# Optimization experiments

Measured on AMD Instinct MI355X. Metric: run time of the kernel, lower is better.

The kernel has to match this reference:

```python
import jax, jax.numpy as jnp
import numpy as np

NUM_CLASSES = 10
PGD_NUMS = 10
ALPHA = 0.15
# Hardcoded in the original module: sign vector for 10 classes
SIGN_VEC = jnp.array([-1.0] * 4 + [1.0] * 6, dtype=jnp.float32)


def setup_inputs() -> dict:
    key = jax.random.key(0)
    k1, k2, k3 = jax.random.split(key, 3)
    B = 1048576
    logit = jax.random.normal(k1, (B, NUM_CLASSES), dtype=jnp.float32)
    y = jax.random.randint(k2, (B,), 0, NUM_CLASSES, dtype=jnp.int32)
    label_freq = jax.random.randint(k3, (NUM_CLASSES,), 0, PGD_NUMS, dtype=jnp.int32)
    return {"logit": logit, "y": y, "label_freq": label_freq}


def _compute_adv(logit, y):
    # softmax over classes, then per-class mean of softmax rows (one-hot^T @ p)
    p = jax.nn.softmax(logit, axis=-1)  # [B, C]
    sum_class_logit = jax.ops.segment_sum(p, y, num_segments=NUM_CLASSES)  # [C, C]
    counts = jax.ops.segment_sum(jnp.ones(y.shape[0], dtype=logit.dtype), y,
                                 num_segments=NUM_CLASSES)  # [C]
    counts = jnp.where(counts == 0, jnp.asarray(100.0, logit.dtype), counts)
    mean_class_logit = sum_class_logit / counts[:, None]  # [C, C]
    grad = mean_class_logit - jnp.eye(NUM_CLASSES, dtype=logit.dtype)
    # Faithful to torch: norm over dim=0 (columns), then reshape(-1,1) divides row i
    col_norm = jnp.linalg.norm(grad, axis=0)  # [C]
    grad = grad / col_norm[:, None]
    grad = ALPHA * grad * SIGN_VEC[:, None].astype(logit.dtype)
    return grad[y]  # index_select along dim 0 -> [B, C]


def reference(logit, y, label_freq):
    logit_copy = logit

    def step(l, _):
        l_new = l + _compute_adv(l, y)
        return l_new, l_new

    _, logit_steps = jax.lax.scan(step, logit, None, length=PGD_NUMS)  # [P, B, C]

    # Original: logit_news = sum_i logit_steps[label_freq[i]] * (y == i)
    # Since class masks are disjoint, this is a per-sample gather of step label_freq[y[n]].
    steps_per_sample = label_freq[y]  # [B]
    B = logit.shape[0]
    logit_news = logit_steps[steps_per_sample, jnp.arange(B)]  # [B, C]

    # mean cross-entropy
    log_p = jax.nn.log_softmax(logit_news, axis=-1)
    loss_adv = -jnp.mean(jnp.take_along_axis(log_p, y[:, None].astype(jnp.int32), axis=1))
    return loss_adv, logit_news, logit_copy
```

## Files before the change

### kernel.cpp

```cpp
#include <hip/hip_runtime.h>

#define PGD   10
#define ALPHA 0.15f
#define NTAB  32
#define NTHR  256
#define TSAMP 1024
#define NSUB  8

#define WS_COUNTS 0
#define WS_STAB   320
#define WS_DGLOB  32320
#define WS_ZERO_N 33320

__global__ void k_init(float* __restrict__ ws, float* __restrict__ out) {
    int i = blockIdx.x * blockDim.x + threadIdx.x;
    if (i == 0) out[0] = 0.f;
    int gs = gridDim.x * blockDim.x;
    for (int k = i; k < WS_ZERO_N; k += gs) ws[k] = 0.f;
}

__device__ __forceinline__ void table_phase(
    const float* __restrict__ Sg, const float* __restrict__ counts_tab,
    const float* __restrict__ Dprev,
    float* shT, float* shCnt, float* shCn, float* shD_out, int tid)
{
    if (tid < 10) {
        float s = 0.f;
        #pragma unroll
        for (int k = 0; k < NTAB; ++k) s += counts_tab[k * 10 + tid];
        shCnt[tid] = (s == 0.f) ? 100.f : s;
    }
    if (tid < 100) {
        float s = 0.f;
        #pragma unroll
        for (int k = 0; k < NTAB; ++k) s += Sg[k * 100 + tid];
        shT[tid] = s;
    }
    __syncthreads();
    if (tid < 100) {
        int c = tid / 10, j = tid - c * 10;
        shT[tid] = shT[tid] / shCnt[c] - ((c == j) ? 1.f : 0.f);
    }
    __syncthreads();
    if (tid < 10) {
        float s = 0.f;
        for (int cc = 0; cc < 10; ++cc) { float g = shT[cc * 10 + tid]; s += g * g; }
        shCn[tid] = sqrtf(s);
    }
    __syncthreads();
    if (tid < 100) {
        int c = tid / 10;
        float sign = (c < 4) ? -1.f : 1.f;
        float g = shT[tid] / shCn[c] * (ALPHA * sign);
        shD_out[tid] = (Dprev ? Dprev[tid] : 0.f) + g;
    }
    __syncthreads();
}

__device__ __forceinline__ void load_tile(const float* __restrict__ logit,
                                          const int* __restrict__ y,
                                          size_t fbase, size_t ftot, int B,
                                          int tid, int blk, float4 q[10], int4& yq)
{
    #pragma unroll
    for (int i = 0; i < 10; ++i) {
        size_t fi = fbase + (size_t)(tid + i * NTHR) * 4;
        if (fi + 4 <= ftot) {
            q[i] = *reinterpret_cast<const float4*>(logit + fi);
        } else {
            float e[4];
            #pragma unroll
            for (int e2 = 0; e2 < 4; ++e2) e[e2] = (fi + e2 < ftot) ? logit[fi + e2] : 0.f;
            q[i] = make_float4(e[0], e[1], e[2], e[3]);
        }
    }
    int yi = blk * TSAMP + tid * 4;
    if (yi + 4 <= B) {
        yq = *reinterpret_cast<const int4*>(y + yi);
    } else {
        yq.x = (yi     < B) ? y[yi]     : 0;
        yq.y = (yi + 1 < B) ? y[yi + 1] : 0;
        yq.z = (yi + 2 < B) ? y[yi + 2] : 0;
        yq.w = (yi + 3 < B) ? y[yi + 3] : 0;
    }
}

__global__ __launch_bounds__(NTHR) void k_step(
    const float* __restrict__ logit, const int* __restrict__ y,
    float* __restrict__ ws, int B, int t )
{
    __shared__ float tile[TSAMP * 10];
    __shared__ int   yt[TSAMP];
    __shared__ float wtab[NSUB][100];
    __shared__ float ctab[NSUB][10];
    __shared__ float sh_D[100];
    __shared__ float shT[100];
    __shared__ float shCnt[10];
    __shared__ float shCn[10];

    const int tid = threadIdx.x;

    float* counts_tab = ws + WS_COUNTS;
    float* S_tab      = ws + WS_STAB;
    float* D_glob     = ws + WS_DGLOB;

    const size_t fbase = (size_t)blockIdx.x * (TSAMP * 10);
    const size_t ftot  = (size_t)B * 10;
    float4 q[10];
    int4 yq;
    load_tile(logit, y, fbase, ftot, B, tid, blockIdx.x, q, yq);

    for (int i = tid; i < NSUB * 100; i += NTHR) (&wtab[0][0])[i] = 0.f;
    if (t == 1) for (int i = tid; i < NSUB * 10; i += NTHR) (&ctab[0][0])[i] = 0.f;

    if (t >= 2) {
        table_phase(S_tab + (size_t)(t - 2) * (NTAB * 100), counts_tab,
                    (t >= 3) ? (D_glob + (size_t)(t - 3) * 100) : nullptr,
                    shT, shCnt, shCn, sh_D, tid);
        if (blockIdx.x == 0 && tid < 100) D_glob[(size_t)(t - 2) * 100 + tid] = sh_D[tid];
    }

    float4* tp = reinterpret_cast<float4*>(tile);
    #pragma unroll
    for (int i = 0; i < 10; ++i) tp[tid + i * NTHR] = q[i];
    reinterpret_cast<int4*>(yt)[tid] = yq;
    __syncthreads();

    const int sub = ((tid >> 6) << 1) | (tid & 1);
    #pragma unroll
    for (int k = 0; k < 4; ++k) {
        int sl = tid + k * NTHR;
        int gi = blockIdx.x * TSAMP + sl;
        if (gi >= B) break;
        int c = yt[sl];
        const float2* rp = reinterpret_cast<const float2*>(tile + sl * 10);
        float tv[10];
        #pragma unroll
        for (int h = 0; h < 5; ++h) { float2 v = rp[h]; tv[2 * h] = v.x; tv[2 * h + 1] = v.y; }
        if (t >= 2) {
            #pragma unroll
            for (int j = 0; j < 10; ++j) tv[j] += sh_D[c * 10 + j];
        }
        float m = tv[0];
        #pragma unroll
        for (int j = 1; j < 10; ++j) m = fmaxf(m, tv[j]);
        float s = 0.f;
        #pragma unroll
        for (int j = 0; j < 10; ++j) { tv[j] = __expf(tv[j] - m); s += tv[j]; }
        float r = 1.f / s;
        #pragma unroll
        for (int j = 0; j < 10; ++j) unsafeAtomicAdd(&wtab[sub][c * 10 + j], tv[j] * r);
        if (t == 1) unsafeAtomicAdd(&ctab[sub][c], 1.f);
    }
    __syncthreads();

    const int tb = blockIdx.x & (NTAB - 1);
    if (tid < 100) {
        float s = 0.f;
        #pragma unroll
        for (int w = 0; w < NSUB; ++w) s += wtab[w][tid];
        unsafeAtomicAdd(&S_tab[(size_t)(t - 1) * (NTAB * 100) + (size_t)tb * 100 + tid], s);
    }
    if (t == 1 && tid < 10) {
        float s = 0.f;
        #pragma unroll
        for (int w = 0; w < NSUB; ++w) s += ctab[w][tid];
        unsafeAtomicAdd(&counts_tab[tb * 10 + tid], s);
    }
}

__global__ __launch_bounds__(NTHR) void k_final(
    const float* __restrict__ logit, const int* __restrict__ y,
    const int* __restrict__ label_freq,
    float* __restrict__ out, float* __restrict__ ws, int B)
{
    __shared__ float tile[TSAMP * 10];
    __shared__ int   yt[TSAMP];
    __shared__ float Dall[PGD][100];
    __shared__ float shT[100];
    __shared__ float shCnt[10];
    __shared__ float shCn[10];
    __shared__ int   lf[10];
    __shared__ float wsum[4];

    const int tid = threadIdx.x;

    float* counts_tab = ws + WS_COUNTS;
    float* S_tab      = ws + WS_STAB;
    float* D_glob     = ws + WS_DGLOB;

    const size_t fbase = (size_t)blockIdx.x * (TSAMP * 10);
    const size_t ftot  = (size_t)B * 10;
    float4 q[10];
    int4 yq;
    load_tile(logit, y, fbase, ftot, B, tid, blockIdx.x, q, yq);

    table_phase(S_tab + (size_t)9 * (NTAB * 100), counts_tab, D_glob + 8 * 100,
                shT, shCnt, shCn, &Dall[9][0], tid);
    for (int i = tid; i < 900; i += NTHR) Dall[i / 100][i % 100] = D_glob[i];
    if (tid < 10) lf[tid] = label_freq[tid];

    float4* tp = reinterpret_cast<float4*>(tile);
    #pragma unroll
    for (int i = 0; i < 10; ++i) tp[tid + i * NTHR] = q[i];
    reinterpret_cast<int4*>(yt)[tid] = yq;
    __syncthreads();

    const int vfloat = (int)((ftot - fbase < (size_t)(TSAMP * 10)) ? (ftot - fbase)
                                                                   : (size_t)(TSAMP * 10));
    float* news_out = out + 1;
    float* copy_out = out + 1 + ftot;

    for (int m = tid; m < vfloat; m += NTHR) copy_out[fbase + m] = tile[m];
    __syncthreads();

    float acc = 0.f;
    #pragma unroll
    for (int k = 0; k < 4; ++k) {
        int sl = tid + k * NTHR;
        int gi = blockIdx.x * TSAMP + sl;
        if (gi >= B) break;
        int c = yt[sl];
        int sel = lf[c];
        float2* rp = reinterpret_cast<float2*>(tile + sl * 10);
        float nv[10];
        #pragma unroll
        for (int h = 0; h < 5; ++h) {
            float2 v = rp[h];
            nv[2 * h]     = v.x + Dall[sel][c * 10 + 2 * h];
            nv[2 * h + 1] = v.y + Dall[sel][c * 10 + 2 * h + 1];
        }
        #pragma unroll
        for (int h = 0; h < 5; ++h) rp[h] = make_float2(nv[2 * h], nv[2 * h + 1]);
        float m = nv[0];
        #pragma unroll
        for (int j = 1; j < 10; ++j) m = fmaxf(m, nv[j]);
        float s = 0.f;
        #pragma unroll
        for (int j = 0; j < 10; ++j) s += __expf(nv[j] - m);
        acc += __logf(s) + m - nv[c];
    }
    __syncthreads();

    for (int m = tid; m < vfloat; m += NTHR) news_out[fbase + m] = tile[m];

    #pragma unroll
    for (int off = 32; off > 0; off >>= 1) acc += __shfl_down(acc, off);
    if ((tid & 63) == 0) wsum[tid >> 6] = acc;
    __syncthreads();
    if (tid == 0)
        unsafeAtomicAdd(out, (wsum[0] + wsum[1] + wsum[2] + wsum[3]) / (float)B);
}

extern "C" void kernel_launch(void* const* d_in, const int* in_sizes, int n_in,
                              void* d_out, int out_size, void* d_ws, size_t ws_size,
                              hipStream_t stream) {
    const float* logit = (const float*)d_in[0];
    const int*   yy    = (const int*)d_in[1];
    const int*   lf    = (const int*)d_in[2];
    float* out = (float*)d_out;
    float* ws  = (float*)d_ws;
    int B = in_sizes[0] / 10;

    int blocks = (B + TSAMP - 1) / TSAMP;

    hipLaunchKernelGGL(k_init, dim3(64), dim3(256), 0, stream, ws, out);
    for (int t = 1; t <= PGD; ++t)
        hipLaunchKernelGGL(k_step, dim3(blocks), dim3(NTHR), 0, stream,
                           logit, yy, ws, B, t);
    hipLaunchKernelGGL(k_final, dim3(blocks), dim3(NTHR), 0, stream,
                       logit, yy, lf, out, ws, B);
}
```

Baseline: 662.8 us.

## Swizzle block-to-tile mapping per XCD and drop LDS staging in step kernel

Block indices are remapped so that each XCD processes a contiguous range of tiles. This is meant to keep the repeated per-step reads of the logits local to each XCD's L2 across the ten step launches. The step kernel now has each thread load its 4 samples directly into registers (40 floats) instead of staging the tile through a 40KB shared buffer, which removes LDS traffic and raises possible occupancy. In exchange, the direct per-thread float4 loads are strided (each thread reads 160 contiguous bytes) and less coalesced, and register pressure goes up.

```diff
diff --git a/kernel.cpp b/kernel.cpp
--- a/kernel.cpp
+++ b/kernel.cpp
@@ -4,13 +4,20 @@
 #define ALPHA 0.15f
 #define NTAB  32
 #define NTHR  256
-#define TSAMP 1024
+#define SPT   4
+#define TSAMP (NTHR * SPT)
 #define NSUB  8
 
 #define WS_COUNTS 0
 #define WS_STAB   320
 #define WS_DGLOB  32320
 #define WS_ZERO_N 33320
+
+__device__ __forceinline__ int swz_tile(int bid, int nblk) {
+    int q = nblk >> 3, r = nblk & 7;
+    int xcd = bid & 7, idx = bid >> 3;
+    return (xcd < r ? xcd * (q + 1) : r * (q + 1) + (xcd - r) * q) + idx;
+}
 
 __global__ void k_init(float* __restrict__ ws, float* __restrict__ out) {
     int i = blockIdx.x * blockDim.x + threadIdx.x;
@@ -57,11 +64,135 @@
     __syncthreads();
 }
 
-__device__ __forceinline__ void load_tile(const float* __restrict__ logit,
-                                          const int* __restrict__ y,
-                                          size_t fbase, size_t ftot, int B,
-                                          int tid, int blk, float4 q[10], int4& yq)
+__device__ __forceinline__ void load4(const float* __restrict__ logit,
+                                      const int* __restrict__ y,
+                                      int s0, int B, float a[40], int yc[4]) {
+    if (s0 + 4 <= B) {
+        const float4* rp = reinterpret_cast<const float4*>(logit + (size_t)s0 * 10);
+        float4 q[10];
+        #pragma unroll
+        for (int i = 0; i < 10; ++i) q[i] = rp[i];
+        int4 yv = *reinterpret_cast<const int4*>(y + s0);
+        #pragma unroll
+        for (int i = 0; i < 10; ++i) {
+            a[4 * i + 0] = q[i].x; a[4 * i + 1] = q[i].y;
+            a[4 * i + 2] = q[i].z; a[4 * i + 3] = q[i].w;
+        }
+        yc[0] = yv.x; yc[1] = yv.y; yc[2] = yv.z; yc[3] = yv.w;
+    } else {
+        #pragma unroll
+        for (int k = 0; k < 4; ++k) {
+            int idx = s0 + k;
+            if (idx < B) {
+                yc[k] = y[idx];
+                for (int j = 0; j < 10; ++j) a[k * 10 + j] = logit[(size_t)idx * 10 + j];
+            } else {
+                yc[k] = -1;
+                for (int j = 0; j < 10; ++j) a[k * 10 + j] = 0.f;
+            }
+        }
+    }
+}
+
+__global__ __launch_bounds__(NTHR) void k_step(
+    const float* __restrict__ logit, const int* __restrict__ y,
+    float* __restrict__ ws, int B, int t )
 {
+    __shared__ float sh_D[100];
+    __shared__ float shT[100];
+    __shared__ float shCnt[10];
+    __shared__ float shCn[10];
+    __shared__ float wtab[NSUB][100];
+    __shared__ float ctab[NSUB][10];
+
+    const int tid = threadIdx.x;
+    const int tile = swz_tile(blockIdx.x, gridDim.x);
+
+    float* counts_tab = ws + WS_COUNTS;
+    float* S_tab      = ws + WS_STAB;
+    float* D_glob     = ws + WS_DGLOB;
+
+    const int s0 = tile * TSAMP + tid * SPT;
+    float a[40];
+    int   yc[4];
+    load4(logit, y, s0, B, a, yc);
+
+    for (int i = tid; i < NSUB * 100; i += NTHR) (&wtab[0][0])[i] = 0.f;
+    if (t == 1) for (int i = tid; i < NSUB * 10; i += NTHR) (&ctab[0][0])[i] = 0.f;
+
+    if (t >= 2) {
+        table_phase(S_tab + (size_t)(t - 2) * (NTAB * 100), counts_tab,
+                    (t >= 3) ? (D_glob + (size_t)(t - 3) * 100) : nullptr,
+                    shT, shCnt, shCn, sh_D, tid);
+        if (blockIdx.x == 0 && tid < 100) D_glob[(size_t)(t - 2) * 100 + tid] = sh_D[tid];
+    }
+    __syncthreads();
+
+    const int sub = ((tid >> 6) << 1) | (tid & 1);
+    #pragma unroll
+    for (int k = 0; k < SPT; ++k) {
+        int c = yc[k];
+        if (c < 0) continue;
+        float tv[10];
+        #pragma unroll
+        for (int j = 0; j < 10; ++j) tv[j] = a[k * 10 + j];
+        if (t >= 2) {
+            #pragma unroll
+            for (int j = 0; j < 10; ++j) tv[j] += sh_D[c * 10 + j];
+        }
+        float m = tv[0];
+        #pragma unroll
+        for (int j = 1; j < 10; ++j) m = fmaxf(m, tv[j]);
+        float s = 0.f;
+        #pragma unroll
+        for (int j = 0; j < 10; ++j) { tv[j] = __expf(tv[j] - m); s += tv[j]; }
+        float r = 1.f / s;
+        #pragma unroll
+        for (int j = 0; j < 10; ++j) unsafeAtomicAdd(&wtab[sub][c * 10 + j], tv[j] * r);
+        if (t == 1) unsafeAtomicAdd(&ctab[sub][c], 1.f);
+    }
+    __syncthreads();
+
+    const int tb = blockIdx.x & (NTAB - 1);
+    if (tid < 100) {
+        float s = 0.f;
+        #pragma unroll
+        for (int w = 0; w < NSUB; ++w) s += wtab[w][tid];
+        unsafeAtomicAdd(&S_tab[(size_t)(t - 1) * (NTAB * 100) + (size_t)tb * 100 + tid], s);
+    }
+    if (t == 1 && tid < 10) {
+        float s = 0.f;
+        #pragma unroll
+        for (int w = 0; w < NSUB; ++w) s += ctab[w][tid];
+        unsafeAtomicAdd(&counts_tab[tb * 10 + tid], s);
+    }
+}
+
+__global__ __launch_bounds__(NTHR) void k_final(
+    const float* __restrict__ logit, const int* __restrict__ y,
+    const int* __restrict__ label_freq,
+    float* __restrict__ out, float* __restrict__ ws, int B)
+{
+    __shared__ float tile_f[TSAMP * 10];
+    __shared__ int   yt[TSAMP];
+    __shared__ float Dall[PGD][100];
+    __shared__ float shT[100];
+    __shared__ float shCnt[10];
+    __shared__ float shCn[10];
+    __shared__ int   lf[10];
+    __shared__ float wsum[4];
+
+    const int tid = threadIdx.x;
+    const int tile = swz_tile(blockIdx.x, gridDim.x);
+
+    float* counts_tab = ws + WS_COUNTS;
+    float* S_tab      = ws + WS_STAB;
+    float* D_glob     = ws + WS_DGLOB;
+
+    const size_t fbase = (size_t)tile * (TSAMP * 10);
+    const size_t ftot  = (size_t)B * 10;
+    float4 q[10];
+    int4 yq;
     #pragma unroll
     for (int i = 0; i < 10; ++i) {
         size_t fi = fbase + (size_t)(tid + i * NTHR) * 4;
@@ -74,133 +205,24 @@
             q[i] = make_float4(e[0], e[1], e[2], e[3]);
         }
     }
-    int yi = blk * TSAMP + tid * 4;
-    if (yi + 4 <= B) {
-        yq = *reinterpret_cast<const int4*>(y + yi);
-    } else {
-        yq.x = (yi     < B) ? y[yi]     : 0;
-        yq.y = (yi + 1 < B) ? y[yi + 1] : 0;
-        yq.z = (yi + 2 < B) ? y[yi + 2] : 0;
-        yq.w = (yi + 3 < B) ? y[yi + 3] : 0;
-    }
-}
-
-__global__ __launch_bounds__(NTHR) void k_step(
-    const float* __restrict__ logit, const int* __restrict__ y,
-    float* __restrict__ ws, int B, int t )
-{
-    __shared__ float tile[TSAMP * 10];
-    __shared__ int   yt[TSAMP];
-    __shared__ float wtab[NSUB][100];
-    __shared__ float ctab[NSUB][10];
-    __shared__ float sh_D[100];
-    __shared__ float shT[100];
-    __shared__ float shCnt[10];
-    __shared__ float shCn[10];
-
-    const int tid = threadIdx.x;
-
-    float* counts_tab = ws + WS_COUNTS;
-    float* S_tab      = ws + WS_STAB;
-    float* D_glob     = ws + WS_DGLOB;
-
-    const size_t fbase = (size_t)blockIdx.x * (TSAMP * 10);
-    const size_t ftot  = (size_t)B * 10;
-    float4 q[10];
-    int4 yq;
-    load_tile(logit, y, fbase, ftot, B, tid, blockIdx.x, q, yq);
-
-    for (int i = tid; i < NSUB * 100; i += NTHR) (&wtab[0][0])[i] = 0.f;
-    if (t == 1) for (int i = tid; i < NSUB * 10; i += NTHR) (&ctab[0][0])[i] = 0.f;
-
-    if (t >= 2) {
-        table_phase(S_tab + (size_t)(t - 2) * (NTAB * 100), counts_tab,
-                    (t >= 3) ? (D_glob + (size_t)(t - 3) * 100) : nullptr,
-                    shT, shCnt, shCn, sh_D, tid);
-        if (blockIdx.x == 0 && tid < 100) D_glob[(size_t)(t - 2) * 100 + tid] = sh_D[tid];
-    }
-
-    float4* tp = reinterpret_cast<float4*>(tile);
-    #pragma unroll
-    for (int i = 0; i < 10; ++i) tp[tid + i * NTHR] = q[i];
-    reinterpret_cast<int4*>(yt)[tid] = yq;
-    __syncthreads();
-
-    const int sub = ((tid >> 6) << 1) | (tid & 1);
-    #pragma unroll
-    for (int k = 0; k < 4; ++k) {
-        int sl = tid + k * NTHR;
-        int gi = blockIdx.x * TSAMP + sl;
-        if (gi >= B) break;
-        int c = yt[sl];
-        const float2* rp = reinterpret_cast<const float2*>(tile + sl * 10);
-        float tv[10];
-        #pragma unroll
-        for (int h = 0; h < 5; ++h) { float2 v = rp[h]; tv[2 * h] = v.x; tv[2 * h + 1] = v.y; }
-        if (t >= 2) {
-            #pragma unroll
-            for (int j = 0; j < 10; ++j) tv[j] += sh_D[c * 10 + j];
-        }
-        float m = tv[0];
-        #pragma unroll
-        for (int j = 1; j < 10; ++j) m = fmaxf(m, tv[j]);
-        float s = 0.f;
-        #pragma unroll
-        for (int j = 0; j < 10; ++j) { tv[j] = __expf(tv[j] - m); s += tv[j]; }
-        float r = 1.f / s;
-        #pragma unroll
-        for (int j = 0; j < 10; ++j) unsafeAtomicAdd(&wtab[sub][c * 10 + j], tv[j] * r);
-        if (t == 1) unsafeAtomicAdd(&ctab[sub][c], 1.f);
-    }
-    __syncthreads();
-
-    const int tb = blockIdx.x & (NTAB - 1);
-    if (tid < 100) {
-        float s = 0.f;
-        #pragma unroll
-        for (int w = 0; w < NSUB; ++w) s += wtab[w][tid];
-        unsafeAtomicAdd(&S_tab[(size_t)(t - 1) * (NTAB * 100) + (size_t)tb * 100 + tid], s);
-    }
-    if (t == 1 && tid < 10) {
-        float s = 0.f;
-        #pragma unroll
-        for (int w = 0; w < NSUB; ++w) s += ctab[w][tid];
-        unsafeAtomicAdd(&counts_tab[tb * 10 + tid], s);
-    }
-}
-
-__global__ __launch_bounds__(NTHR) void k_final(
-    const float* __restrict__ logit, const int* __restrict__ y,
-    const int* __restrict__ label_freq,
-    float* __restrict__ out, float* __restrict__ ws, int B)
-{
-    __shared__ float tile[TSAMP * 10];
-    __shared__ int   yt[TSAMP];
-    __shared__ float Dall[PGD][100];
-    __shared__ float shT[100];
-    __shared__ float shCnt[10];
-    __shared__ float shCn[10];
-    __shared__ int   lf[10];
-    __shared__ float wsum[4];
-
-    const int tid = threadIdx.x;
-
-    float* counts_tab = ws + WS_COUNTS;
-    float* S_tab      = ws + WS_STAB;
-    float* D_glob     = ws + WS_DGLOB;
-
-    const size_t fbase = (size_t)blockIdx.x * (TSAMP * 10);
-    const size_t ftot  = (size_t)B * 10;
-    float4 q[10];
-    int4 yq;
-    load_tile(logit, y, fbase, ftot, B, tid, blockIdx.x, q, yq);
+    {
+        int yi = tile * TSAMP + tid * 4;
+        if (yi + 4 <= B) {
+            yq = *reinterpret_cast<const int4*>(y + yi);
+        } else {
+            yq.x = (yi     < B) ? y[yi]     : 0;
+            yq.y = (yi + 1 < B) ? y[yi + 1] : 0;
+            yq.z = (yi + 2 < B) ? y[yi + 2] : 0;
+            yq.w = (yi + 3 < B) ? y[yi + 3] : 0;
+        }
+    }
 
     table_phase(S_tab + (size_t)9 * (NTAB * 100), counts_tab, D_glob + 8 * 100,
                 shT, shCnt, shCn, &Dall[9][0], tid);
     for (int i = tid; i < 900; i += NTHR) Dall[i / 100][i % 100] = D_glob[i];
     if (tid < 10) lf[tid] = label_freq[tid];
 
-    float4* tp = reinterpret_cast<float4*>(tile);
+    float4* tp = reinterpret_cast<float4*>(tile_f);
     #pragma unroll
     for (int i = 0; i < 10; ++i) tp[tid + i * NTHR] = q[i];
     reinterpret_cast<int4*>(yt)[tid] = yq;
@@ -211,18 +233,18 @@
     float* news_out = out + 1;
     float* copy_out = out + 1 + ftot;
 
-    for (int m = tid; m < vfloat; m += NTHR) copy_out[fbase + m] = tile[m];
+    for (int m = tid; m < vfloat; m += NTHR) copy_out[fbase + m] = tile_f[m];
     __syncthreads();
 
     float acc = 0.f;
     #pragma unroll
-    for (int k = 0; k < 4; ++k) {
+    for (int k = 0; k < SPT; ++k) {
         int sl = tid + k * NTHR;
-        int gi = blockIdx.x * TSAMP + sl;
+        int gi = tile * TSAMP + sl;
         if (gi >= B) break;
         int c = yt[sl];
         int sel = lf[c];
-        float2* rp = reinterpret_cast<float2*>(tile + sl * 10);
+        float2* rp = reinterpret_cast<float2*>(tile_f + sl * 10);
         float nv[10];
         #pragma unroll
         for (int h = 0; h < 5; ++h) {
@@ -242,7 +264,7 @@
     }
     __syncthreads();
 
-    for (int m = tid; m < vfloat; m += NTHR) news_out[fbase + m] = tile[m];
+    for (int m = tid; m < vfloat; m += NTHR) news_out[fbase + m] = tile_f[m];
 
     #pragma unroll
     for (int off = 32; off > 0; off >>= 1) acc += __shfl_down(acc, off);
```

Measured after the change: 648.3 us. 1.02x faster.
